# Optimization experiments

Measured on AMD Instinct MI355X. Metric: run time of the kernel, lower is better.

## Reference

```python
import jax, jax.numpy as jnp
import numpy as np

NHID = 512
T_K, T_Q, B = 256, 128, 8


def setup_inputs() -> dict:
    key = jax.random.key(0)
    k1, k2, k3, k4, k5 = jax.random.split(key, 5)
    query = jax.random.normal(k1, (T_Q, B, NHID), dtype=jnp.float32)
    c_key = jax.random.normal(k2, (T_K, B, NHID), dtype=jnp.float32)
    mask = jax.random.randint(k3, (T_K, B), 0, 2).astype(bool)
    # att_mlp params: Linear(2*nhid, nhid) -> Tanh -> Linear(nhid, 1)
    # stored as [in, out] so y = x @ W + b (torch Linear weight transposed)
    W1 = jax.random.normal(k4, (2 * NHID, NHID), dtype=jnp.float32) / np.sqrt(2 * NHID)
    b1 = jnp.zeros((NHID,), dtype=jnp.float32)
    W2 = jax.random.normal(k5, (NHID, 1), dtype=jnp.float32) / np.sqrt(NHID)
    b2 = jnp.zeros((1,), dtype=jnp.float32)
    return {"query": query, "c_key": c_key, "mask": mask,
            "W1": W1, "b1": b1, "W2": W2, "b2": b2}


def reference(query, c_key, mask, W1, b1, W2, b2):
    H = query.shape[-1]
    # cat([k_expand, q_expand], -1) @ W1 == k @ W1[:H] + q @ W1[H:]
    # (avoids materializing the [T_k, T_q, B, 2H] concat the torch code builds)
    k_proj = jnp.einsum('kbh,hd->kbd', c_key, W1[:H])   # [T_k, B, H]
    q_proj = jnp.einsum('qbh,hd->qbd', query, W1[H:])   # [T_q, B, H]
    h = jnp.tanh(k_proj[:, None, :, :] + q_proj[None, :, :, :] + b1)  # [T_k, T_q, B, H]
    att_score = jnp.einsum('kqbh,ho->kqb', h, W2) + b2[0]             # [T_k, T_q, B]
    att_score = jnp.where(mask[:, None, :], -jnp.inf, att_score)
    att_prob = jax.nn.softmax(att_score, axis=0)                      # softmax over keys
    # c_val defaults to c_key in the original forward
    ant_vec = jnp.einsum('kqb,kbh->qbh', att_prob, c_key)             # [T_q, B, H]
    return ant_vec, att_prob
```

## Files before the change

kernel.cpp:

```cpp
#include <hip/hip_runtime.h>
#include <math.h>

#define NHID 512
#define T_K  256
#define T_Q  128
#define BB   8

constexpr float C2L2E = 2.8853900817779268f;
constexpr float L2E   = 1.4426950408889634f;

__device__ __forceinline__ float fexp2(float x) { return __builtin_amdgcn_exp2f(x); }
__device__ __forceinline__ float frcp(float x)  { return __builtin_amdgcn_rcpf(x); }

typedef __attribute__((ext_vector_type(8))) short bf16x8;
typedef __attribute__((ext_vector_type(4))) float f32x4;

__device__ __forceinline__ unsigned short f2bf(float x) {
    unsigned u = __builtin_bit_cast(unsigned, x);
    unsigned r = (u + 0x7FFFu + ((u >> 16) & 1u)) >> 16;
    return (unsigned short)r;
}
__device__ __forceinline__ float bf2f(unsigned short h) {
    unsigned u = ((unsigned)h) << 16;
    return __builtin_bit_cast(float, u);
}
__device__ __forceinline__ unsigned packbf(float a, float b) {
    return (unsigned)f2bf(a) | ((unsigned)f2bf(b) << 16);
}
__device__ __forceinline__ float lo16(unsigned u) {
    return __builtin_bit_cast(float, u << 16);
}
__device__ __forceinline__ float hi16(unsigned u) {
    return __builtin_bit_cast(float, u & 0xFFFF0000u);
}

__global__ __launch_bounds__(256) void proj_kernel(
    const float* __restrict__ qry, const float* __restrict__ ckey,
    const float* __restrict__ W1, const float* __restrict__ b1,
    uint4* __restrict__ ekto, float* __restrict__ eq,
    unsigned int* __restrict__ ckp)
{
    const int row0 = blockIdx.x * 32;
    const int col0 = blockIdx.y * 64;
    const bool isK = row0 < 2048;
    const int bhalf = isK ? 0 : 512;

    __shared__ __align__(16) unsigned short As_h[32 * 64];
    __shared__ __align__(16) unsigned short As_l[32 * 64];
    __shared__ __align__(16) unsigned short Bs_h[64 * 64];
    __shared__ __align__(16) unsigned short Bs_l[64 * 64];

    const int t    = threadIdx.x;
    const int wave = t >> 6;
    const int lane = t & 63;
    const int wm = (wave & 1) * 16;
    const int wn = (wave >> 1) * 32;

    f32x4 acc[2] = {};

    const int srA = t >> 3;
    const int scA = (t & 7) * 8;
    const float* gA = (isK ? ckey + (size_t)(row0 + srA) * 512
                           : qry  + (size_t)(row0 - 2048 + srA) * 512) + scA;
    const int swA = ((scA >> 3) ^ (srA & 7)) * 8;
    const bool emit_ckp = isK && (col0 == 0);
    const int rowA = row0 + srA;
    unsigned int* ckp_dst = emit_ckp
        ? ckp + ((size_t)(rowA & 7) * 256 + (rowA >> 3)) * 256
        : nullptr;

    const int nB = t & 63;
    const int kgB = wave * 16;
    const float* gB = W1 + (size_t)(bhalf + kgB) * 512 + col0 + nB;
    const int caB = wave * 2;
    const int swB0 = nB * 64 + (((caB + 0) ^ (nB & 7)) * 8);
    const int swB1 = nB * 64 + (((caB + 1) ^ (nB & 7)) * 8);

    const int quad = lane >> 4, fr = lane & 15;

    float4 pa0 = *(const float4*)&gA[0];
    float4 pa1 = *(const float4*)&gA[4];
    float bv[16];
    #pragma unroll
    for (int kk = 0; kk < 16; ++kk)
        bv[kk] = gB[(size_t)kk * 512];

    for (int k0 = 0; k0 < 512; k0 += 64) {
        float fa[8];
        *(float4*)&fa[0] = pa0; *(float4*)&fa[4] = pa1;
        union { uint4 v; unsigned short s[8]; } hA, lA, bh0, bh1, bl0, bl1;
        #pragma unroll
        for (int e = 0; e < 8; ++e) {
            const unsigned short hb = f2bf(fa[e]);
            hA.s[e] = hb; lA.s[e] = f2bf(fa[e] - bf2f(hb));
        }
        #pragma unroll
        for (int e = 0; e < 8; ++e) {
            const unsigned short hb = f2bf(bv[e]);
            bh0.s[e] = hb; bl0.s[e] = f2bf(bv[e] - bf2f(hb));
        }
        #pragma unroll
        for (int e = 0; e < 8; ++e) {
            const unsigned short hb = f2bf(bv[8 + e]);
            bh1.s[e] = hb; bl1.s[e] = f2bf(bv[8 + e] - bf2f(hb));
        }
        if (emit_ckp)
            *(uint4*)&ckp_dst[(k0 + scA) >> 1] = hA.v;

        __syncthreads();
        *(uint4*)&As_h[srA * 64 + swA] = hA.v;
        *(uint4*)&As_l[srA * 64 + swA] = lA.v;
        *(uint4*)&Bs_h[swB0] = bh0.v;  *(uint4*)&Bs_h[swB1] = bh1.v;
        *(uint4*)&Bs_l[swB0] = bl0.v;  *(uint4*)&Bs_l[swB1] = bl1.v;
        __syncthreads();

        if (k0 + 64 < 512) {
            pa0 = *(const float4*)&gA[k0 + 64];
            pa1 = *(const float4*)&gA[k0 + 68];
            #pragma unroll
            for (int kk = 0; kk < 16; ++kk)
                bv[kk] = gB[(size_t)(k0 + 64 + kk) * 512];
        }

        #pragma unroll
        for (int ks = 0; ks < 2; ++ks) {
            const int cchunk = ks * 4 + quad;
            const int m = wm + fr;
            const bf16x8 afh = *(const bf16x8*)&As_h[m * 64 + ((cchunk ^ (m & 7)) * 8)];
            const bf16x8 afl = *(const bf16x8*)&As_l[m * 64 + ((cchunk ^ (m & 7)) * 8)];
            bf16x8 bfh[2], bfl[2];
            #pragma unroll
            for (int nt = 0; nt < 2; ++nt) {
                const int n = wn + nt * 16 + fr;
                bfh[nt] = *(const bf16x8*)&Bs_h[n * 64 + ((cchunk ^ (n & 7)) * 8)];
                bfl[nt] = *(const bf16x8*)&Bs_l[n * 64 + ((cchunk ^ (n & 7)) * 8)];
            }
            #pragma unroll
            for (int nt = 0; nt < 2; ++nt) {
                acc[nt] = __builtin_amdgcn_mfma_f32_16x16x32_bf16(afh, bfh[nt], acc[nt], 0, 0, 0);
                acc[nt] = __builtin_amdgcn_mfma_f32_16x16x32_bf16(afh, bfl[nt], acc[nt], 0, 0, 0);
                acc[nt] = __builtin_amdgcn_mfma_f32_16x16x32_bf16(afl, bfh[nt], acc[nt], 0, 0, 0);
            }
        }
    }

    #pragma unroll
    for (int nt = 0; nt < 2; ++nt) {
        const int colg = col0 + wn + nt * 16 + fr;
        const float b1v = b1[colg];
        #pragma unroll
        for (int i = 0; i < 4; ++i) {
            const int rowg = row0 + wm + quad * 4 + i;
            const float v = acc[nt][i];
            if (isK) {
                const float e = fexp2((v + b1v) * C2L2E);
                const float ep = __shfl_xor(e, 1, 64);
                unsigned pk = ((fr & 1) == 0) ? packbf(e, ep) : packbf(ep, e);
                unsigned pk2 = __shfl_xor(pk, 2, 64);
                if (fr & 2) { unsigned tmp = pk; pk = pk2; pk2 = tmp; }
                const unsigned px  = __shfl_xor(pk, 4, 64);
                const unsigned px2 = __shfl_xor(pk2, 4, 64);
                if ((fr & 7) == 0) {
                    const int kidx = rowg >> 3;
                    const int bb   = rowg & 7;
                    const int ho   = colg >> 3;
                    ekto[((size_t)bb * 64 + ho) * 256 + kidx] =
                        make_uint4(pk, pk2, px, px2);
                }
            } else {
                eq[(size_t)(rowg - 2048) * 512 + colg] = fexp2(v * C2L2E);
            }
        }
    }
}

__global__ __launch_bounds__(512, 4) void scoreav_kernel(
    const uint4* __restrict__ ekto, const float* __restrict__ eq,
    const float* __restrict__ W2, const float* __restrict__ b2,
    const int* __restrict__ mask, const unsigned int* __restrict__ ckp,
    float* __restrict__ prob_out, float* __restrict__ out_ant)
{
    const int t    = threadIdx.x;
    const int lane = t & 63;
    const int wave = __builtin_amdgcn_readfirstlane(t >> 6);
    const int kk   = t & 255;
    const int half = t >> 8;
    const int q0   = blockIdx.x * 2;
    const int b    = blockIdx.y;

    __shared__ float eq0s[512], eq1s[512], w2s[512];
    __shared__ float rp[2][512];
    __shared__ float ps[2][256];

    eq0s[t] = eq[((size_t)q0 * 8 + b) * 512 + t];
    eq1s[t] = eq[((size_t)(q0 + 1) * 8 + b) * 512 + t];
    w2s[t]  = W2[t];

    const float4 wA = *(const float4*)&W2[lane * 4];
    const float4 wB = *(const float4*)&W2[256 + lane * 4];
    float s2 = wA.x + wA.y + wA.z + wA.w + wB.x + wB.y + wB.z + wB.w;
    #pragma unroll
    for (int m = 32; m; m >>= 1) s2 += __shfl_xor(s2, m, 64);
    const float base = s2 + b2[0];
    __syncthreads();

    const uint4* __restrict__ ekb = ekto + (size_t)b * 64 * 256 + kk;
    float r0a = 0.f, r0b = 0.f, r1a = 0.f, r1b = 0.f;

    uint4 LA0, LA1, LA2, LA3, LB0, LB1, LB2, LB3;

#define PREF(D, G) \
    D##0 = ekb[(size_t)(half * 32 + (G) * 4 + 0) * 256]; \
    D##1 = ekb[(size_t)(half * 32 + (G) * 4 + 1) * 256]; \
    D##2 = ekb[(size_t)(half * 32 + (G) * 4 + 2) * 256]; \
    D##3 = ekb[(size_t)(half * 32 + (G) * 4 + 3) * 256];

#define JBODY(U, G, J) { \
    const int h = (half * 32 + (G) * 4 + (J)) * 8; \
    const float ek0 = lo16(U.x), ek1 = hi16(U.x); \
    const float ek2 = lo16(U.y), ek3 = hi16(U.y); \
    const float ek4 = lo16(U.z), ek5 = hi16(U.z); \
    const float ek6 = lo16(U.w), ek7 = hi16(U.w); \
    const float4 wL = *(const float4*)&w2s[h]; \
    const float4 wH = *(const float4*)&w2s[h + 4]; \
    {  \
        const float4 eL = *(const float4*)&eq0s[h]; \
        const float4 eH = *(const float4*)&eq0s[h + 4]; \
        { \
            const float a0 = fmaf(ek0, eL.x, 1.0f); \
            const float a1 = fmaf(ek1, eL.y, 1.0f); \
            const float a2 = fmaf(ek2, eL.z, 1.0f); \
            const float a3 = fmaf(ek3, eL.w, 1.0f); \
            const float d01 = a0 * a1, d23 = a2 * a3; \
            const float n01 = fmaf(wL.x, a1, wL.y * a0); \
            const float n23 = fmaf(wL.z, a3, wL.w * a2); \
            const float N = fmaf(n01, d23, n23 * d01); \
            r0a = fmaf(N, frcp(d01 * d23), r0a); \
        } \
        { \
            const float a0 = fmaf(ek4, eH.x, 1.0f); \
            const float a1 = fmaf(ek5, eH.y, 1.0f); \
            const float a2 = fmaf(ek6, eH.z, 1.0f); \
            const float a3 = fmaf(ek7, eH.w, 1.0f); \
            const float d01 = a0 * a1, d23 = a2 * a3; \
            const float n01 = fmaf(wH.x, a1, wH.y * a0); \
            const float n23 = fmaf(wH.z, a3, wH.w * a2); \
            const float N = fmaf(n01, d23, n23 * d01); \
            r0b = fmaf(N, frcp(d01 * d23), r0b); \
        } \
    } \
    {  \
        const float4 eL = *(const float4*)&eq1s[h]; \
        const float4 eH = *(const float4*)&eq1s[h + 4]; \
        { \
            const float a0 = fmaf(ek0, eL.x, 1.0f); \
            const float a1 = fmaf(ek1, eL.y, 1.0f); \
            const float a2 = fmaf(ek2, eL.z, 1.0f); \
            const float a3 = fmaf(ek3, eL.w, 1.0f); \
            const float d01 = a0 * a1, d23 = a2 * a3; \
            const float n01 = fmaf(wL.x, a1, wL.y * a0); \
            const float n23 = fmaf(wL.z, a3, wL.w * a2); \
            const float N = fmaf(n01, d23, n23 * d01); \
            r1a = fmaf(N, frcp(d01 * d23), r1a); \
        } \
        { \
            const float a0 = fmaf(ek4, eH.x, 1.0f); \
            const float a1 = fmaf(ek5, eH.y, 1.0f); \
            const float a2 = fmaf(ek6, eH.z, 1.0f); \
            const float a3 = fmaf(ek7, eH.w, 1.0f); \
            const float d01 = a0 * a1, d23 = a2 * a3; \
            const float n01 = fmaf(wH.x, a1, wH.y * a0); \
            const float n23 = fmaf(wH.z, a3, wH.w * a2); \
            const float N = fmaf(n01, d23, n23 * d01); \
            r1b = fmaf(N, frcp(d01 * d23), r1b); \
        } \
    } \
}

#define GROUP(D, G) JBODY(D##0, G, 0) JBODY(D##1, G, 1) JBODY(D##2, G, 2) JBODY(D##3, G, 3)

    PREF(LA, 0)
    PREF(LB, 1) GROUP(LA, 0)
    PREF(LA, 2) GROUP(LB, 1)
    PREF(LB, 3) GROUP(LA, 2)
    PREF(LA, 4) GROUP(LB, 3)
    PREF(LB, 5) GROUP(LA, 4)
    PREF(LA, 6) GROUP(LB, 5)
    PREF(LB, 7) GROUP(LA, 6)
                GROUP(LB, 7)

#undef GROUP
#undef JBODY
#undef PREF

    rp[0][t] = r0a + r0b;
    rp[1][t] = r1a + r1b;
    __syncthreads();

    if (t < 256) {
        const int msk = mask[t * 8 + b];
        float s0 = base - 2.0f * (rp[0][t] + rp[0][t + 256]);
        float s1 = base - 2.0f * (rp[1][t] + rp[1][t + 256]);
        if (msk) { s0 = -INFINITY; s1 = -INFINITY; }
        ps[0][t] = s0;
        ps[1][t] = s1;
    }
    __syncthreads();

    if (wave < 2) {
        float4 sv = *(const float4*)&ps[wave][lane * 4];
        float m = fmaxf(fmaxf(sv.x, sv.y), fmaxf(sv.z, sv.w));
        #pragma unroll
        for (int d = 32; d; d >>= 1) m = fmaxf(m, __shfl_xor(m, d, 64));
        float4 pv;
        pv.x = fexp2((sv.x - m) * L2E);
        pv.y = fexp2((sv.y - m) * L2E);
        pv.z = fexp2((sv.z - m) * L2E);
        pv.w = fexp2((sv.w - m) * L2E);
        float sum = pv.x + pv.y + pv.z + pv.w;
        #pragma unroll
        for (int d = 32; d; d >>= 1) sum += __shfl_xor(sum, d, 64);
        const float inv = frcp(sum);
        pv.x *= inv; pv.y *= inv; pv.z *= inv; pv.w *= inv;
        *(float4*)&ps[wave][lane * 4] = pv;
        const int qb_idx = (q0 + wave) * 8 + b;
        const int kbase = lane * 4;
        prob_out[(size_t)(kbase + 0) * 1024 + qb_idx] = pv.x;
        prob_out[(size_t)(kbase + 1) * 1024 + qb_idx] = pv.y;
        prob_out[(size_t)(kbase + 2) * 1024 + qb_idx] = pv.z;
        prob_out[(size_t)(kbase + 3) * 1024 + qb_idx] = pv.w;
    }
    __syncthreads();

    {
        const int kq = lane >> 3;
        const int hq = lane & 7;
        const int pbase = wave * 32 + hq * 4;
        const unsigned int* __restrict__ ckb = ckp + (size_t)b * 256 * 256;
        float4 a0q0 = {}, a1q0 = {}, a0q1 = {}, a1q1 = {};
        #pragma unroll 8
        for (int ki = 0; ki < 32; ++ki) {
            const int k = ki * 8 + kq;
            const uint4 U = *(const uint4*)&ckb[(size_t)k * 256 + pbase];
            const float c0 = lo16(U.x), c1 = hi16(U.x);
            const float c2 = lo16(U.y), c3 = hi16(U.y);
            const float c4 = lo16(U.z), c5 = hi16(U.z);
            const float c6 = lo16(U.w), c7 = hi16(U.w);
            const float p0 = ps[0][k];
            const float p1 = ps[1][k];
            a0q0.x = fmaf(p0, c0, a0q0.x); a0q0.y = fmaf(p0, c1, a0q0.y);
            a0q0.z = fmaf(p0, c2, a0q0.z); a0q0.w = fmaf(p0, c3, a0q0.w);
            a1q0.x = fmaf(p0, c4, a1q0.x); a1q0.y = fmaf(p0, c5, a1q0.y);
            a1q0.z = fmaf(p0, c6, a1q0.z); a1q0.w = fmaf(p0, c7, a1q0.w);
            a0q1.x = fmaf(p1, c0, a0q1.x); a0q1.y = fmaf(p1, c1, a0q1.y);
            a0q1.z = fmaf(p1, c2, a0q1.z); a0q1.w = fmaf(p1, c3, a0q1.w);
            a1q1.x = fmaf(p1, c4, a1q1.x); a1q1.y = fmaf(p1, c5, a1q1.y);
            a1q1.z = fmaf(p1, c6, a1q1.z); a1q1.w = fmaf(p1, c7, a1q1.w);
        }
        #pragma unroll
        for (int d = 8; d <= 32; d <<= 1) {
            a0q0.x += __shfl_xor(a0q0.x, d, 64); a0q0.y += __shfl_xor(a0q0.y, d, 64);
            a0q0.z += __shfl_xor(a0q0.z, d, 64); a0q0.w += __shfl_xor(a0q0.w, d, 64);
            a1q0.x += __shfl_xor(a1q0.x, d, 64); a1q0.y += __shfl_xor(a1q0.y, d, 64);
            a1q0.z += __shfl_xor(a1q0.z, d, 64); a1q0.w += __shfl_xor(a1q0.w, d, 64);
            a0q1.x += __shfl_xor(a0q1.x, d, 64); a0q1.y += __shfl_xor(a0q1.y, d, 64);
            a0q1.z += __shfl_xor(a0q1.z, d, 64); a0q1.w += __shfl_xor(a0q1.w, d, 64);
            a1q1.x += __shfl_xor(a1q1.x, d, 64); a1q1.y += __shfl_xor(a1q1.y, d, 64);
            a1q1.z += __shfl_xor(a1q1.z, d, 64); a1q1.w += __shfl_xor(a1q1.w, d, 64);
        }
        if (lane < 8) {
            const int h0 = wave * 64 + hq * 8;
            float* o0 = &out_ant[((size_t)q0 * 8 + b) * 512 + h0];
            float* o1 = &out_ant[((size_t)(q0 + 1) * 8 + b) * 512 + h0];
            *(float4*)&o0[0] = a0q0;  *(float4*)&o0[4] = a1q0;
            *(float4*)&o1[0] = a0q1;  *(float4*)&o1[4] = a1q1;
        }
    }
}

extern "C" void kernel_launch(void* const* d_in, const int* in_sizes, int n_in,
                              void* d_out, int out_size, void* d_ws, size_t ws_size,
                              hipStream_t stream)
{
    const float* qry  = (const float*)d_in[0];
    const float* ckey = (const float*)d_in[1];
    const int*   mask = (const int*)d_in[2];
    const float* W1   = (const float*)d_in[3];
    const float* b1   = (const float*)d_in[4];
    const float* W2   = (const float*)d_in[5];
    const float* b2   = (const float*)d_in[6];

    float* out_ant  = (float*)d_out;
    float* out_prob = (float*)d_out + T_Q * BB * NHID;

    float* ws = (float*)d_ws;
    uint4* ws_ekto = (uint4*)ws;
    float* ws_eq  = ws + 524288;
    unsigned int* ws_ckp = (unsigned int*)(ws + 1048576);

    proj_kernel<<<dim3(96, 8), 256, 0, stream>>>(qry, ckey, W1, b1,
                                                 ws_ekto, ws_eq, ws_ckp);
    scoreav_kernel<<<dim3(64, 8), 512, 0, stream>>>(ws_ekto, ws_eq, W2, b2, mask, ws_ckp,
                                                    out_prob, out_ant);
}
```

Measured before the change: 109.6 us.

## Pack per-query values as float2 pairs to use packed FMA in score and AV loops

Interleaves the two queries' exp(q) values into float2 shared-memory pairs and rewrites the score and attention-value loops with 2-wide vector FMA/mul. On CDNA3/4 this can lower to v_pk_fma_f32, roughly halving the VALU instruction count in the compute-bound inner loops. W2 is now read straight from global memory as scalar loads (hu is wave-uniform) instead of from LDS. The probabilities are also stored in an interleaved layout for the AV stage. Output stores become scalar, and the packed ops may need extra register moves to build the broadcast operands.

Result: no change. 109.9 us (median of 2 runs) (+0.2%).

```diff
diff --git a/kernel.cpp b/kernel.cpp
--- a/kernel.cpp
+++ b/kernel.cpp
@@ -14,6 +14,12 @@
 
 typedef __attribute__((ext_vector_type(8))) short bf16x8;
 typedef __attribute__((ext_vector_type(4))) float f32x4;
+typedef __attribute__((ext_vector_type(2))) float f32x2;
+typedef __attribute__((ext_vector_type(4))) float f32x4v;
+
+__device__ __forceinline__ f32x2 fma2(f32x2 a, f32x2 b, f32x2 c) {
+    return __builtin_elementwise_fma(a, b, c);
+}
 
 __device__ __forceinline__ unsigned short f2bf(float x) {
     unsigned u = __builtin_bit_cast(unsigned, x);
@@ -183,18 +189,22 @@
     const int t    = threadIdx.x;
     const int lane = t & 63;
     const int wave = __builtin_amdgcn_readfirstlane(t >> 6);
+    const int hu   = __builtin_amdgcn_readfirstlane(t >> 8);
     const int kk   = t & 255;
-    const int half = t >> 8;
     const int q0   = blockIdx.x * 2;
     const int b    = blockIdx.y;
 
-    __shared__ float eq0s[512], eq1s[512], w2s[512];
-    __shared__ float rp[2][512];
+    __shared__ __align__(16) f32x2 eqp[512];
+    __shared__ __align__(16) f32x2 rp2[512];
     __shared__ float ps[2][256];
-
-    eq0s[t] = eq[((size_t)q0 * 8 + b) * 512 + t];
-    eq1s[t] = eq[((size_t)(q0 + 1) * 8 + b) * 512 + t];
-    w2s[t]  = W2[t];
+    __shared__ __align__(8) f32x2 ps2[256];
+
+    {
+        const float* eqr0 = eq + ((size_t)q0 * 8 + b) * 512;
+        const float* eqr1 = eq + ((size_t)(q0 + 1) * 8 + b) * 512;
+        f32x2 ep; ep.x = eqr0[t]; ep.y = eqr1[t];
+        eqp[t] = ep;
+    }
 
     const float4 wA = *(const float4*)&W2[lane * 4];
     const float4 wB = *(const float4*)&W2[256 + lane * 4];
@@ -205,75 +215,56 @@
     __syncthreads();
 
     const uint4* __restrict__ ekb = ekto + (size_t)b * 64 * 256 + kk;
-    float r0a = 0.f, r0b = 0.f, r1a = 0.f, r1b = 0.f;
+    const f32x2 one2 = {1.0f, 1.0f};
+    f32x2 ra = {0.f, 0.f}, rb = {0.f, 0.f};
 
     uint4 LA0, LA1, LA2, LA3, LB0, LB1, LB2, LB3;
 
 #define PREF(D, G) \
-    D##0 = ekb[(size_t)(half * 32 + (G) * 4 + 0) * 256]; \
-    D##1 = ekb[(size_t)(half * 32 + (G) * 4 + 1) * 256]; \
-    D##2 = ekb[(size_t)(half * 32 + (G) * 4 + 2) * 256]; \
-    D##3 = ekb[(size_t)(half * 32 + (G) * 4 + 3) * 256];
+    D##0 = ekb[(size_t)(hu * 32 + (G) * 4 + 0) * 256]; \
+    D##1 = ekb[(size_t)(hu * 32 + (G) * 4 + 1) * 256]; \
+    D##2 = ekb[(size_t)(hu * 32 + (G) * 4 + 2) * 256]; \
+    D##3 = ekb[(size_t)(hu * 32 + (G) * 4 + 3) * 256];
 
 #define JBODY(U, G, J) { \
-    const int h = (half * 32 + (G) * 4 + (J)) * 8; \
+    const int hw = (hu * 32 + (G) * 4 + (J)) * 8; \
     const float ek0 = lo16(U.x), ek1 = hi16(U.x); \
     const float ek2 = lo16(U.y), ek3 = hi16(U.y); \
     const float ek4 = lo16(U.z), ek5 = hi16(U.z); \
     const float ek6 = lo16(U.w), ek7 = hi16(U.w); \
-    const float4 wL = *(const float4*)&w2s[h]; \
-    const float4 wH = *(const float4*)&w2s[h + 4]; \
-    {  \
-        const float4 eL = *(const float4*)&eq0s[h]; \
-        const float4 eH = *(const float4*)&eq0s[h + 4]; \
-        { \
-            const float a0 = fmaf(ek0, eL.x, 1.0f); \
-            const float a1 = fmaf(ek1, eL.y, 1.0f); \
-            const float a2 = fmaf(ek2, eL.z, 1.0f); \
-            const float a3 = fmaf(ek3, eL.w, 1.0f); \
-            const float d01 = a0 * a1, d23 = a2 * a3; \
-            const float n01 = fmaf(wL.x, a1, wL.y * a0); \
-            const float n23 = fmaf(wL.z, a3, wL.w * a2); \
-            const float N = fmaf(n01, d23, n23 * d01); \
-            r0a = fmaf(N, frcp(d01 * d23), r0a); \
-        } \
-        { \
-            const float a0 = fmaf(ek4, eH.x, 1.0f); \
-            const float a1 = fmaf(ek5, eH.y, 1.0f); \
-            const float a2 = fmaf(ek6, eH.z, 1.0f); \
-            const float a3 = fmaf(ek7, eH.w, 1.0f); \
-            const float d01 = a0 * a1, d23 = a2 * a3; \
-            const float n01 = fmaf(wH.x, a1, wH.y * a0); \
-            const float n23 = fmaf(wH.z, a3, wH.w * a2); \
-            const float N = fmaf(n01, d23, n23 * d01); \
-            r0b = fmaf(N, frcp(d01 * d23), r0b); \
-        } \
+    const f32x4v E01 = *(const f32x4v*)&eqp[hw]; \
+    const f32x4v E23 = *(const f32x4v*)&eqp[hw + 2]; \
+    const f32x4v E45 = *(const f32x4v*)&eqp[hw + 4]; \
+    const f32x4v E67 = *(const f32x4v*)&eqp[hw + 6]; \
+    const float w0 = W2[hw + 0], w1 = W2[hw + 1]; \
+    const float w2v = W2[hw + 2], w3 = W2[hw + 3]; \
+    const float w4 = W2[hw + 4], w5 = W2[hw + 5]; \
+    const float w6 = W2[hw + 6], w7 = W2[hw + 7]; \
+    { \
+        const f32x2 a0 = fma2((f32x2){ek0, ek0}, (f32x2){E01.x, E01.y}, one2); \
+        const f32x2 a1 = fma2((f32x2){ek1, ek1}, (f32x2){E01.z, E01.w}, one2); \
+        const f32x2 a2 = fma2((f32x2){ek2, ek2}, (f32x2){E23.x, E23.y}, one2); \
+        const f32x2 a3 = fma2((f32x2){ek3, ek3}, (f32x2){E23.z, E23.w}, one2); \
+        const f32x2 d01 = a0 * a1, d23 = a2 * a3; \
+        const f32x2 n01 = fma2((f32x2){w0, w0}, a1, (f32x2){w1, w1} * a0); \
+        const f32x2 n23 = fma2((f32x2){w2v, w2v}, a3, (f32x2){w3, w3} * a2); \
+        const f32x2 N = fma2(n01, d23, n23 * d01); \
+        const f32x2 D = d01 * d23; \
+        const f32x2 R = {frcp(D.x), frcp(D.y)}; \
+        ra = fma2(N, R, ra); \
     } \
-    {  \
-        const float4 eL = *(const float4*)&eq1s[h]; \
-        const float4 eH = *(const float4*)&eq1s[h + 4]; \
-        { \
-            const float a0 = fmaf(ek0, eL.x, 1.0f); \
-            const float a1 = fmaf(ek1, eL.y, 1.0f); \
-            const float a2 = fmaf(ek2, eL.z, 1.0f); \
-            const float a3 = fmaf(ek3, eL.w, 1.0f); \
-            const float d01 = a0 * a1, d23 = a2 * a3; \
-            const float n01 = fmaf(wL.x, a1, wL.y * a0); \
-            const float n23 = fmaf(wL.z, a3, wL.w * a2); \
-            const float N = fmaf(n01, d23, n23 * d01); \
-            r1a = fmaf(N, frcp(d01 * d23), r1a); \
-        } \
-        { \
-            const float a0 = fmaf(ek4, eH.x, 1.0f); \
-            const float a1 = fmaf(ek5, eH.y, 1.0f); \
-            const float a2 = fmaf(ek6, eH.z, 1.0f); \
-            const float a3 = fmaf(ek7, eH.w, 1.0f); \
-            const float d01 = a0 * a1, d23 = a2 * a3; \
-            const float n01 = fmaf(wH.x, a1, wH.y * a0); \
-            const float n23 = fmaf(wH.z, a3, wH.w * a2); \
-            const float N = fmaf(n01, d23, n23 * d01); \
-            r1b = fmaf(N, frcp(d01 * d23), r1b); \
-        } \
+    { \
+        const f32x2 a0 = fma2((f32x2){ek4, ek4}, (f32x2){E45.x, E45.y}, one2); \
+        const f32x2 a1 = fma2((f32x2){ek5, ek5}, (f32x2){E45.z, E45.w}, one2); \
+        const f32x2 a2 = fma2((f32x2){ek6, ek6}, (f32x2){E67.x, E67.y}, one2); \
+        const f32x2 a3 = fma2((f32x2){ek7, ek7}, (f32x2){E67.z, E67.w}, one2); \
+        const f32x2 d01 = a0 * a1, d23 = a2 * a3; \
+        const f32x2 n01 = fma2((f32x2){w4, w4}, a1, (f32x2){w5, w5} * a0); \
+        const f32x2 n23 = fma2((f32x2){w6, w6}, a3, (f32x2){w7, w7} * a2); \
+        const f32x2 N = fma2(n01, d23, n23 * d01); \
+        const f32x2 D = d01 * d23; \
+        const f32x2 R = {frcp(D.x), frcp(D.y)}; \
+        rb = fma2(N, R, rb); \
     } \
 }
 
@@ -293,14 +284,14 @@
 #undef JBODY
 #undef PREF
 
-    rp[0][t] = r0a + r0b;
-    rp[1][t] = r1a + r1b;
+    rp2[t] = ra + rb;
     __syncthreads();
 
     if (t < 256) {
         const int msk = mask[t * 8 + b];
-        float s0 = base - 2.0f * (rp[0][t] + rp[0][t + 256]);
-        float s1 = base - 2.0f * (rp[1][t] + rp[1][t + 256]);
+        const f32x2 rsum = rp2[t] + rp2[t + 256];
+        float s0 = base - 2.0f * rsum.x;
+        float s1 = base - 2.0f * rsum.y;
         if (msk) { s0 = -INFINITY; s1 = -INFINITY; }
         ps[0][t] = s0;
         ps[1][t] = s1;
@@ -322,7 +313,11 @@
         for (int d = 32; d; d >>= 1) sum += __shfl_xor(sum, d, 64);
         const float inv = frcp(sum);
         pv.x *= inv; pv.y *= inv; pv.z *= inv; pv.w *= inv;
-        *(float4*)&ps[wave][lane * 4] = pv;
+        float* p2f = (float*)ps2;
+        p2f[(lane * 4 + 0) * 2 + wave] = pv.x;
+        p2f[(lane * 4 + 1) * 2 + wave] = pv.y;
+        p2f[(lane * 4 + 2) * 2 + wave] = pv.z;
+        p2f[(lane * 4 + 3) * 2 + wave] = pv.w;
         const int qb_idx = (q0 + wave) * 8 + b;
         const int kbase = lane * 4;
         prob_out[(size_t)(kbase + 0) * 1024 + qb_idx] = pv.x;
@@ -337,7 +332,7 @@
         const int hq = lane & 7;
         const int pbase = wave * 32 + hq * 4;
         const unsigned int* __restrict__ ckb = ckp + (size_t)b * 256 * 256;
-        float4 a0q0 = {}, a1q0 = {}, a0q1 = {}, a1q1 = {};
+        f32x2 a0 = {}, a1 = {}, a2 = {}, a3 = {}, a4 = {}, a5 = {}, a6 = {}, a7 = {};
         #pragma unroll 8
         for (int ki = 0; ki < 32; ++ki) {
             const int k = ki * 8 + kq;
@@ -346,34 +341,35 @@
             const float c2 = lo16(U.y), c3 = hi16(U.y);
             const float c4 = lo16(U.z), c5 = hi16(U.z);
             const float c6 = lo16(U.w), c7 = hi16(U.w);
-            const float p0 = ps[0][k];
-            const float p1 = ps[1][k];
-            a0q0.x = fmaf(p0, c0, a0q0.x); a0q0.y = fmaf(p0, c1, a0q0.y);
-            a0q0.z = fmaf(p0, c2, a0q0.z); a0q0.w = fmaf(p0, c3, a0q0.w);
-            a1q0.x = fmaf(p0, c4, a1q0.x); a1q0.y = fmaf(p0, c5, a1q0.y);
-            a1q0.z = fmaf(p0, c6, a1q0.z); a1q0.w = fmaf(p0, c7, a1q0.w);
-            a0q1.x = fmaf(p1, c0, a0q1.x); a0q1.y = fmaf(p1, c1, a0q1.y);
-            a0q1.z = fmaf(p1, c2, a0q1.z); a0q1.w = fmaf(p1, c3, a0q1.w);
-            a1q1.x = fmaf(p1, c4, a1q1.x); a1q1.y = fmaf(p1, c5, a1q1.y);
-            a1q1.z = fmaf(p1, c6, a1q1.z); a1q1.w = fmaf(p1, c7, a1q1.w);
+            const f32x2 p = ps2[k];
+            a0 = fma2(p, (f32x2){c0, c0}, a0);
+            a1 = fma2(p, (f32x2){c1, c1}, a1);
+            a2 = fma2(p, (f32x2){c2, c2}, a2);
+            a3 = fma2(p, (f32x2){c3, c3}, a3);
+            a4 = fma2(p, (f32x2){c4, c4}, a4);
+            a5 = fma2(p, (f32x2){c5, c5}, a5);
+            a6 = fma2(p, (f32x2){c6, c6}, a6);
+            a7 = fma2(p, (f32x2){c7, c7}, a7);
         }
         #pragma unroll
         for (int d = 8; d <= 32; d <<= 1) {
-            a0q0.x += __shfl_xor(a0q0.x, d, 64); a0q0.y += __shfl_xor(a0q0.y, d, 64);
-            a0q0.z += __shfl_xor(a0q0.z, d, 64); a0q0.w += __shfl_xor(a0q0.w, d, 64);
-            a1q0.x += __shfl_xor(a1q0.x, d, 64); a1q0.y += __shfl_xor(a1q0.y, d, 64);
-            a1q0.z += __shfl_xor(a1q0.z, d, 64); a1q0.w += __shfl_xor(a1q0.w, d, 64);
-            a0q1.x += __shfl_xor(a0q1.x, d, 64); a0q1.y += __shfl_xor(a0q1.y, d, 64);
-            a0q1.z += __shfl_xor(a0q1.z, d, 64); a0q1.w += __shfl_xor(a0q1.w, d, 64);
-            a1q1.x += __shfl_xor(a1q1.x, d, 64); a1q1.y += __shfl_xor(a1q1.y, d, 64);
-            a1q1.z += __shfl_xor(a1q1.z, d, 64); a1q1.w += __shfl_xor(a1q1.w, d, 64);
+            a0.x += __shfl_xor(a0.x, d, 64); a0.y += __shfl_xor(a0.y, d, 64);
+            a1.x += __shfl_xor(a1.x, d, 64); a1.y += __shfl_xor(a1.y, d, 64);
+            a2.x += __shfl_xor(a2.x, d, 64); a2.y += __shfl_xor(a2.y, d, 64);
+            a3.x += __shfl_xor(a3.x, d, 64); a3.y += __shfl_xor(a3.y, d, 64);
+            a4.x += __shfl_xor(a4.x, d, 64); a4.y += __shfl_xor(a4.y, d, 64);
+            a5.x += __shfl_xor(a5.x, d, 64); a5.y += __shfl_xor(a5.y, d, 64);
+            a6.x += __shfl_xor(a6.x, d, 64); a6.y += __shfl_xor(a6.y, d, 64);
+            a7.x += __shfl_xor(a7.x, d, 64); a7.y += __shfl_xor(a7.y, d, 64);
         }
         if (lane < 8) {
             const int h0 = wave * 64 + hq * 8;
             float* o0 = &out_ant[((size_t)q0 * 8 + b) * 512 + h0];
             float* o1 = &out_ant[((size_t)(q0 + 1) * 8 + b) * 512 + h0];
-            *(float4*)&o0[0] = a0q0;  *(float4*)&o0[4] = a1q0;
-            *(float4*)&o1[0] = a0q1;  *(float4*)&o1[4] = a1q1;
+            o0[0] = a0.x; o0[1] = a1.x; o0[2] = a2.x; o0[3] = a3.x;
+            o0[4] = a4.x; o0[5] = a5.x; o0[6] = a6.x; o0[7] = a7.x;
+            o1[0] = a0.y; o1[1] = a1.y; o1[2] = a2.y; o1[3] = a3.y;
+            o1[4] = a4.y; o1[5] = a5.y; o1[6] = a6.y; o1[7] = a7.y;
         }
     }
 }
```
